# Kernel tuning notes

Measured on AMD Instinct MI355X. Metric: run time of the kernel, lower is better.

## Reference

```python
import jax, jax.numpy as jnp
import numpy as np

DIM = 256
MUL = 4
NUM_ENTRIES = 64
B, K = 16, 64
R = MUL * DIM


def setup_inputs() -> dict:
    key = jax.random.key(0)
    k_slots, k_idx, k_w1, k_w2 = jax.random.split(key, 4)
    slots = jax.random.normal(k_slots, (B, K, DIM), dtype=jnp.float32)
    indices = jax.random.randint(k_idx, (B, K), 0, NUM_ENTRIES, dtype=jnp.int64)
    # xavier_normal: std = sqrt(2 / (fan_in + fan_out)) over last two dims
    std1 = float(np.sqrt(2.0 / (DIM + R)))
    std2 = float(np.sqrt(2.0 / (R + DIM)))
    w1 = jax.random.normal(k_w1, (NUM_ENTRIES, DIM, R), dtype=jnp.float32) * std1
    w2 = jax.random.normal(k_w2, (NUM_ENTRIES, R, DIM), dtype=jnp.float32) * std2
    b1 = jnp.zeros((NUM_ENTRIES, R), dtype=jnp.float32)
    b2 = jnp.zeros((NUM_ENTRIES, DIM), dtype=jnp.float32)
    return {"slots": slots, "w1": w1, "b1": b1, "w2": w2, "b2": b2, "indices": indices}


def reference(slots, w1, b1, w2, b2, indices):
    # gather per-(b,k) expert weights, then 2-layer MLP (matvec per slot)
    h = jnp.einsum('bkd,bkdr->bkr', slots, w1[indices]) + b1[indices]  # (B,K,R)
    h = jax.nn.relu(h)
    out = jnp.einsum('bkr,bkrd->bkd', h, w2[indices]) + b2[indices]    # (B,K,DIM)
    return out
```

## Files before the change

kernel.cpp:

```cpp
#include <hip/hip_runtime.h>
#include <stdint.h>

#define DIMC 256
#define RTOT 1024
#define NE 64
#define NSLOT 1024
#define RCN 8
#define RCW 128
#define TILE 32
#define XSTR 264
#define KS1 8
#define KS2 4
#define NTW2 2

typedef short bfrag __attribute__((ext_vector_type(8)));
typedef float f32x4 __attribute__((ext_vector_type(4)));

__global__ __launch_bounds__(1024) void bucket_kernel(
    const int* __restrict__ idx, int* __restrict__ count,
    int* __restrict__ start, int* __restrict__ list) {
  __shared__ int cnt[NE];
  __shared__ int offs[NE];
  __shared__ int cur[NE];
  int t = threadIdx.x;
  if (t < NE) cnt[t] = 0;
  __syncthreads();
  int e = idx[t] & (NE - 1);
  atomicAdd(&cnt[e], 1);
  __syncthreads();
  if (t == 0) {
    int acc = 0;
    for (int i = 0; i < NE; ++i) { offs[i] = acc; cur[i] = acc; acc += cnt[i]; }
  }
  __syncthreads();
  if (t < NE) { count[t] = cnt[t]; start[t] = offs[t]; }
  int pos = atomicAdd(&cur[e], 1);
  list[pos] = t;
}

static __device__ __forceinline__ unsigned short f2bf(float f) {
  unsigned u = __float_as_uint(f);
  return (unsigned short)((u + 0x7FFFu + ((u >> 16) & 1u)) >> 16);
}

static __device__ __forceinline__ bfrag pack8(const float* f) {
  union { unsigned short u[8]; bfrag v; } r;
#pragma unroll
  for (int i = 0; i < 8; ++i) r.u[i] = f2bf(f[i]);
  return r.v;
}

__global__ __launch_bounds__(512) void mlp_kernel(
    const float* __restrict__ slots, const float* __restrict__ w1,
    const float* __restrict__ b1, const float* __restrict__ w2,
    const float* __restrict__ b2, const int* __restrict__ count,
    const int* __restrict__ start, const int* __restrict__ list,
    float* __restrict__ out) {
  const int rc = blockIdx.x;
  const int e  = blockIdx.y;
  const int n  = count[e];
  if (n == 0) return;
  const int t  = threadIdx.x;
  const int l  = t & 63;
  const int w  = t >> 6;
  const int ln = l & 15;
  const int kg = l >> 4;
  const int rbase = rc * RCW;
  const int st = start[e];

  __shared__ unsigned short X[TILE * XSTR];
  __shared__ int sid[TILE];

  const float* w1e = w1 + (size_t)e * DIMC * RTOT + rbase;
  const float* w2e = w2 + (size_t)e * RTOT * DIMC + (size_t)rbase * DIMC;

  for (int s0 = 0; s0 < n; s0 += TILE) {
    const int m = (n - s0 < TILE) ? (n - s0) : TILE;

    __syncthreads();
    if (t < TILE) sid[t] = (t < m) ? list[st + s0 + t] : 0;
    __syncthreads();

    for (int i = t; i < TILE * 64; i += 512) {
      int s = i >> 6, d4 = (i & 63) * 4;
      float4 v = make_float4(0.f, 0.f, 0.f, 0.f);
      if (s < m) v = ((const float4*)slots)[(size_t)sid[s] * 64 + (i & 63)];
      union { unsigned short u[4]; uint2 q; } p;
      p.u[0] = f2bf(v.x); p.u[1] = f2bf(v.y);
      p.u[2] = f2bf(v.z); p.u[3] = f2bf(v.w);
      *(uint2*)&X[s * XSTR + d4] = p.q;
    }
    __syncthreads();

    f32x4 acc1[2];
    acc1[0] = (f32x4)(0.f); acc1[1] = (f32x4)(0.f);
    {
      const int col = w * 16 + ln;
      float bc[8], bn[8];
#pragma unroll
      for (int j = 0; j < 8; ++j)
        bc[j] = w1e[(size_t)(kg * 8 + j) * RTOT + col];

#pragma unroll
      for (int ks = 0; ks < KS1; ++ks) {
        if (ks + 1 < KS1) {
          const int kb = (ks + 1) * 32;
#pragma unroll
          for (int j = 0; j < 8; ++j)
            bn[j] = w1e[(size_t)(kb + kg * 8 + j) * RTOT + col];
        }
        const unsigned short* xp = &X[(size_t)ln * XSTR + ks * 32 + kg * 8];
        bfrag a0 = *(const bfrag*)xp;
        bfrag a1 = *(const bfrag*)(xp + 16 * XSTR);
        bfrag b = pack8(bc);
        acc1[0] = __builtin_amdgcn_mfma_f32_16x16x32_bf16(a0, b, acc1[0], 0, 0, 0);
        acc1[1] = __builtin_amdgcn_mfma_f32_16x16x32_bf16(a1, b, acc1[1], 0, 0, 0);
#pragma unroll
        for (int j = 0; j < 8; ++j) bc[j] = bn[j];
      }
    }

    __syncthreads();

    {
      const int col = w * 16 + ln;
      const float b1v = b1[e * RTOT + rbase + col];
#pragma unroll
      for (int mt = 0; mt < 2; ++mt)
#pragma unroll
        for (int reg = 0; reg < 4; ++reg) {
          float h = fmaxf(acc1[mt][reg] + b1v, 0.f);
          X[(mt * 16 + kg * 4 + reg) * XSTR + col] = f2bf(h);
        }
    }
    __syncthreads();

    f32x4 acc2[2][NTW2];
#pragma unroll
    for (int mt = 0; mt < 2; ++mt)
#pragma unroll
      for (int nt = 0; nt < NTW2; ++nt) acc2[mt][nt] = (f32x4)(0.f);
    {
      float bc[NTW2][8], bn[NTW2][8];
#pragma unroll
      for (int nt = 0; nt < NTW2; ++nt)
#pragma unroll
        for (int j = 0; j < 8; ++j)
          bc[nt][j] = w2e[(size_t)(kg * 8 + j) * DIMC + w * 32 + nt * 16 + ln];

#pragma unroll
      for (int ks = 0; ks < KS2; ++ks) {
        if (ks + 1 < KS2) {
          const int kb = (ks + 1) * 32;
#pragma unroll
          for (int nt = 0; nt < NTW2; ++nt)
#pragma unroll
            for (int j = 0; j < 8; ++j)
              bn[nt][j] = w2e[(size_t)(kb + kg * 8 + j) * DIMC + w * 32 + nt * 16 + ln];
        }
        const unsigned short* xp = &X[(size_t)ln * XSTR + ks * 32 + kg * 8];
        bfrag a0 = *(const bfrag*)xp;
        bfrag a1 = *(const bfrag*)(xp + 16 * XSTR);
#pragma unroll
        for (int nt = 0; nt < NTW2; ++nt) {
          bfrag b = pack8(bc[nt]);
          acc2[0][nt] = __builtin_amdgcn_mfma_f32_16x16x32_bf16(a0, b, acc2[0][nt], 0, 0, 0);
          acc2[1][nt] = __builtin_amdgcn_mfma_f32_16x16x32_bf16(a1, b, acc2[1][nt], 0, 0, 0);
        }
#pragma unroll
        for (int nt = 0; nt < NTW2; ++nt)
#pragma unroll
          for (int j = 0; j < 8; ++j) bc[nt][j] = bn[nt][j];
      }
    }

#pragma unroll
    for (int nt = 0; nt < NTW2; ++nt) {
      const int col = w * 32 + nt * 16 + ln;
      const float b2v = (rc == 0) ? b2[e * DIMC + col] : 0.f;
#pragma unroll
      for (int mt = 0; mt < 2; ++mt)
#pragma unroll
        for (int reg = 0; reg < 4; ++reg) {
          const int row = mt * 16 + kg * 4 + reg;
          if (row < m)
            atomicAdd(&out[(size_t)sid[row] * DIMC + col], acc2[mt][nt][reg] + b2v);
        }
    }
  }
}

extern "C" void kernel_launch(void* const* d_in, const int* in_sizes, int n_in,
                              void* d_out, int out_size, void* d_ws, size_t ws_size,
                              hipStream_t stream) {
  const float* slots   = (const float*)d_in[0];
  const float* w1      = (const float*)d_in[1];
  const float* b1      = (const float*)d_in[2];
  const float* w2      = (const float*)d_in[3];
  const float* b2      = (const float*)d_in[4];
  const int*   indices = (const int*)d_in[5];
  float* out = (float*)d_out;

  int* ws    = (int*)d_ws;
  int* count = ws;
  int* start = ws + 64;
  int* list  = ws + 128;

  hipMemsetAsync(d_out, 0, (size_t)out_size * sizeof(float), stream);
  bucket_kernel<<<1, NSLOT, 0, stream>>>(indices, count, start, list);
  mlp_kernel<<<dim3(RCN, NE), 512, 0, stream>>>(slots, w1, b1, w2, b2,
                                                count, start, list, out);
}
```

Baseline: 170.3 us.

## Fuse bucketing into MLP kernel and triple-buffer weights via global_load_lds

```diff
diff --git a/kernel.cpp b/kernel.cpp
--- a/kernel.cpp
+++ b/kernel.cpp
@@ -9,34 +9,17 @@
 #define RCW 128
 #define TILE 32
 #define XSTR 264
-#define KS1 8
-#define KS2 4
-#define NTW2 2
+#define NT 16
 
 typedef short bfrag __attribute__((ext_vector_type(8)));
 typedef float f32x4 __attribute__((ext_vector_type(4)));
 
-__global__ __launch_bounds__(1024) void bucket_kernel(
-    const int* __restrict__ idx, int* __restrict__ count,
-    int* __restrict__ start, int* __restrict__ list) {
-  __shared__ int cnt[NE];
-  __shared__ int offs[NE];
-  __shared__ int cur[NE];
-  int t = threadIdx.x;
-  if (t < NE) cnt[t] = 0;
-  __syncthreads();
-  int e = idx[t] & (NE - 1);
-  atomicAdd(&cnt[e], 1);
-  __syncthreads();
-  if (t == 0) {
-    int acc = 0;
-    for (int i = 0; i < NE; ++i) { offs[i] = acc; cur[i] = acc; acc += cnt[i]; }
-  }
-  __syncthreads();
-  if (t < NE) { count[t] = cnt[t]; start[t] = offs[t]; }
-  int pos = atomicAdd(&cur[e], 1);
-  list[pos] = t;
-}
+#define VMCNT(N) asm volatile("s_waitcnt vmcnt(" #N ")" ::: "memory")
+#define LGKM0_BAR()                                          \
+  do {                                                       \
+    asm volatile("s_waitcnt lgkmcnt(0)" ::: "memory");       \
+    __builtin_amdgcn_s_barrier();                            \
+  } while (0)
 
 static __device__ __forceinline__ unsigned short f2bf(float f) {
   unsigned u = __float_as_uint(f);
@@ -50,37 +33,71 @@
   return r.v;
 }
 
-__global__ __launch_bounds__(512) void mlp_kernel(
+static __device__ __forceinline__ void gload16(const float* g, float* l) {
+  __builtin_amdgcn_global_load_lds(
+      (const __attribute__((address_space(1))) void*)g,
+      (__attribute__((address_space(3))) void*)l, 16, 0, 0);
+}
+
+__global__ __launch_bounds__(512, 4) void mlp_kernel(
     const float* __restrict__ slots, const float* __restrict__ w1,
     const float* __restrict__ b1, const float* __restrict__ w2,
-    const float* __restrict__ b2, const int* __restrict__ count,
-    const int* __restrict__ start, const int* __restrict__ list,
+    const float* __restrict__ b2, const int* __restrict__ indices,
     float* __restrict__ out) {
   const int rc = blockIdx.x;
   const int e  = blockIdx.y;
-  const int n  = count[e];
-  if (n == 0) return;
   const int t  = threadIdx.x;
   const int l  = t & 63;
   const int w  = t >> 6;
   const int ln = l & 15;
   const int kg = l >> 4;
   const int rbase = rc * RCW;
-  const int st = start[e];
 
-  __shared__ unsigned short X[TILE * XSTR];
+  __shared__ __align__(16) float WT[3][4096];
+  __shared__ __align__(16) unsigned short X[TILE * XSTR];
+  __shared__ int blist[NSLOT];
   __shared__ int sid[TILE];
+  __shared__ int bn_s;
+
+  if (t == 0) bn_s = 0;
+  __syncthreads();
+  {
+    int i0 = indices[t] & (NE - 1);
+    int i1 = indices[t + 512] & (NE - 1);
+    if (i0 == e) { int p = atomicAdd(&bn_s, 1); blist[p] = t; }
+    if (i1 == e) { int p = atomicAdd(&bn_s, 1); blist[p] = t + 512; }
+  }
+  __syncthreads();
+  const int n = bn_s;
+  if (n == 0) return;
 
   const float* w1e = w1 + (size_t)e * DIMC * RTOT + rbase;
   const float* w2e = w2 + (size_t)e * RTOT * DIMC + (size_t)rbase * DIMC;
+  const int   c    = w * 16 + ln;
+  const float b1v  = b1[e * RTOT + rbase + c];
+
+  auto STAGE = [&](int tt, float* buf) {
+    if (tt < 8) {
+      const float* g = w1e + (size_t)(tt * 32 + (t >> 5)) * RTOT + (t & 31) * 4;
+      gload16(g, buf + t * 4);
+      gload16(g + (size_t)16 * RTOT, buf + 2048 + t * 4);
+    } else {
+      const int rt = (tt - 8) >> 1, dh = tt & 1;
+      const float* g =
+          w2e + (size_t)(rt * 32 + (t >> 5)) * DIMC + dh * 128 + (t & 31) * 4;
+      gload16(g, buf + t * 4);
+      gload16(g + 16 * DIMC, buf + 2048 + t * 4);
+    }
+  };
 
   for (int s0 = 0; s0 < n; s0 += TILE) {
     const int m = (n - s0 < TILE) ? (n - s0) : TILE;
 
-    __syncthreads();
-    if (t < TILE) sid[t] = (t < m) ? list[st + s0 + t] : 0;
-    __syncthreads();
+    LGKM0_BAR();
+    if (t < TILE) sid[t] = (t < m) ? blist[s0 + t] : 0;
+    LGKM0_BAR();
 
+#pragma unroll
     for (int i = t; i < TILE * 64; i += 512) {
       int s = i >> 6, d4 = (i & 63) * 4;
       float4 v = make_float4(0.f, 0.f, 0.f, 0.f);
@@ -90,93 +107,63 @@
       p.u[2] = f2bf(v.z); p.u[3] = f2bf(v.w);
       *(uint2*)&X[s * XSTR + d4] = p.q;
     }
-    __syncthreads();
 
     f32x4 acc1[2];
     acc1[0] = (f32x4)(0.f); acc1[1] = (f32x4)(0.f);
-    {
-      const int col = w * 16 + ln;
-      float bc[8], bn[8];
-#pragma unroll
-      for (int j = 0; j < 8; ++j)
-        bc[j] = w1e[(size_t)(kg * 8 + j) * RTOT + col];
-
-#pragma unroll
-      for (int ks = 0; ks < KS1; ++ks) {
-        if (ks + 1 < KS1) {
-          const int kb = (ks + 1) * 32;
-#pragma unroll
-          for (int j = 0; j < 8; ++j)
-            bn[j] = w1e[(size_t)(kb + kg * 8 + j) * RTOT + col];
-        }
-        const unsigned short* xp = &X[(size_t)ln * XSTR + ks * 32 + kg * 8];
-        bfrag a0 = *(const bfrag*)xp;
-        bfrag a1 = *(const bfrag*)(xp + 16 * XSTR);
-        bfrag b = pack8(bc);
-        acc1[0] = __builtin_amdgcn_mfma_f32_16x16x32_bf16(a0, b, acc1[0], 0, 0, 0);
-        acc1[1] = __builtin_amdgcn_mfma_f32_16x16x32_bf16(a1, b, acc1[1], 0, 0, 0);
-#pragma unroll
-        for (int j = 0; j < 8; ++j) bc[j] = bn[j];
-      }
-    }
-
-    __syncthreads();
-
-    {
-      const int col = w * 16 + ln;
-      const float b1v = b1[e * RTOT + rbase + col];
-#pragma unroll
-      for (int mt = 0; mt < 2; ++mt)
-#pragma unroll
-        for (int reg = 0; reg < 4; ++reg) {
-          float h = fmaxf(acc1[mt][reg] + b1v, 0.f);
-          X[(mt * 16 + kg * 4 + reg) * XSTR + col] = f2bf(h);
-        }
-    }
-    __syncthreads();
-
-    f32x4 acc2[2][NTW2];
+    f32x4 acc2[2][2];
 #pragma unroll
     for (int mt = 0; mt < 2; ++mt)
 #pragma unroll
-      for (int nt = 0; nt < NTW2; ++nt) acc2[mt][nt] = (f32x4)(0.f);
-    {
-      float bc[NTW2][8], bn[NTW2][8];
-#pragma unroll
-      for (int nt = 0; nt < NTW2; ++nt)
-#pragma unroll
-        for (int j = 0; j < 8; ++j)
-          bc[nt][j] = w2e[(size_t)(kg * 8 + j) * DIMC + w * 32 + nt * 16 + ln];
+      for (int dh = 0; dh < 2; ++dh) acc2[mt][dh] = (f32x4)(0.f);
+
+    STAGE(0, WT[0]);
+    STAGE(1, WT[1]);
 
 #pragma unroll
-      for (int ks = 0; ks < KS2; ++ks) {
-        if (ks + 1 < KS2) {
-          const int kb = (ks + 1) * 32;
+    for (int tt = 0; tt < NT; ++tt) {
+      if (tt + 2 < NT) STAGE(tt + 2, WT[(tt + 2) % 3]);
+
+      if (tt == 8) {
 #pragma unroll
-          for (int nt = 0; nt < NTW2; ++nt)
+        for (int mt = 0; mt < 2; ++mt)
 #pragma unroll
-            for (int j = 0; j < 8; ++j)
-              bn[nt][j] = w2e[(size_t)(kb + kg * 8 + j) * DIMC + w * 32 + nt * 16 + ln];
+          for (int reg = 0; reg < 4; ++reg) {
+            float h = fmaxf(acc1[mt][reg] + b1v, 0.f);
+            X[(mt * 16 + kg * 4 + reg) * XSTR + c] = f2bf(h);
+          }
+      }
+
+      if (tt < NT - 2)       VMCNT(4);
+      else if (tt == NT - 2) VMCNT(2);
+      else                   VMCNT(0);
+      LGKM0_BAR();
+
+      {
+        const float* buf = WT[tt % 3];
+        float f[8];
+#pragma unroll
+        for (int j = 0; j < 8; ++j) f[j] = buf[(kg * 8 + j) * RCW + c];
+        bfrag b = pack8(f);
+        if (tt < 8) {
+          bfrag a0 = *(const bfrag*)&X[ln * XSTR + tt * 32 + kg * 8];
+          bfrag a1 = *(const bfrag*)&X[(16 + ln) * XSTR + tt * 32 + kg * 8];
+          acc1[0] = __builtin_amdgcn_mfma_f32_16x16x32_bf16(a0, b, acc1[0], 0, 0, 0);
+          acc1[1] = __builtin_amdgcn_mfma_f32_16x16x32_bf16(a1, b, acc1[1], 0, 0, 0);
+        } else {
+          const int rt = (tt - 8) >> 1, dh = tt & 1;
+          bfrag a0 = *(const bfrag*)&X[ln * XSTR + rt * 32 + kg * 8];
+          bfrag a1 = *(const bfrag*)&X[(16 + ln) * XSTR + rt * 32 + kg * 8];
+          acc2[0][dh] = __builtin_amdgcn_mfma_f32_16x16x32_bf16(a0, b, acc2[0][dh], 0, 0, 0);
+          acc2[1][dh] = __builtin_amdgcn_mfma_f32_16x16x32_bf16(a1, b, acc2[1][dh], 0, 0, 0);
         }
-        const unsigned short* xp = &X[(size_t)ln * XSTR + ks * 32 + kg * 8];
-        bfrag a0 = *(const bfrag*)xp;
-        bfrag a1 = *(const bfrag*)(xp + 16 * XSTR);
-#pragma unroll
-        for (int nt = 0; nt < NTW2; ++nt) {
-          bfrag b = pack8(bc[nt]);
-          acc2[0][nt] = __builtin_amdgcn_mfma_f32_16x16x32_bf16(a0, b, acc2[0][nt], 0, 0, 0);
-          acc2[1][nt] = __builtin_amdgcn_mfma_f32_16x16x32_bf16(a1, b, acc2[1][nt], 0, 0, 0);
-        }
-#pragma unroll
-        for (int nt = 0; nt < NTW2; ++nt)
-#pragma unroll
-          for (int j = 0; j < 8; ++j) bc[nt][j] = bn[nt][j];
       }
+
+      LGKM0_BAR();
     }
 
 #pragma unroll
-    for (int nt = 0; nt < NTW2; ++nt) {
-      const int col = w * 32 + nt * 16 + ln;
+    for (int dh = 0; dh < 2; ++dh) {
+      const int col = dh * 128 + c;
       const float b2v = (rc == 0) ? b2[e * DIMC + col] : 0.f;
 #pragma unroll
       for (int mt = 0; mt < 2; ++mt)
@@ -184,7 +171,8 @@
         for (int reg = 0; reg < 4; ++reg) {
           const int row = mt * 16 + kg * 4 + reg;
           if (row < m)
-            atomicAdd(&out[(size_t)sid[row] * DIMC + col], acc2[mt][nt][reg] + b2v);
+            atomicAdd(&out[(size_t)sid[row] * DIMC + col],
+                      acc2[mt][dh][reg] + b2v);
         }
     }
   }
@@ -201,13 +189,9 @@
   const int*   indices = (const int*)d_in[5];
   float* out = (float*)d_out;
 
-  int* ws    = (int*)d_ws;
-  int* count = ws;
-  int* start = ws + 64;
-  int* list  = ws + 128;
+  (void)d_ws; (void)ws_size;
 
   hipMemsetAsync(d_out, 0, (size_t)out_size * sizeof(float), stream);
-  bucket_kernel<<<1, NSLOT, 0, stream>>>(indices, count, start, list);
   mlp_kernel<<<dim3(RCN, NE), 512, 0, stream>>>(slots, w1, b1, w2, b2,
-                                                count, start, list, out);
+                                                indices, out);
 }
```

Measured after the change: 172.6 us. Within noise of the previous version (+1.4%).
